# Kernel optimization log

Hardware: AMD Instinct MI355X
Metric: run time of the kernel (lower is better)

## Reference

```python
import jax, jax.numpy as jnp
from jax import lax
import numpy as np

H = 64   # hidden_dim
R = 32   # rank


def setup_inputs() -> dict:
    key = jax.random.key(0)
    ks = jax.random.split(key, 18)
    B, C, T = 64, 256, 512
    s = 0.1
    f32 = jnp.float32
    return {
        "x": jax.random.normal(ks[0], (B, C, T), f32),
        "y": jax.random.normal(ks[1], (B, C, 1), f32),
        # GRU layer 0 (input_size=1)
        "W_ih0": (jax.random.normal(ks[2], (3 * H, 1), f32) * s),
        "W_hh0": (jax.random.normal(ks[3], (3 * H, H), f32) * s),
        "b_ih0": (jax.random.normal(ks[4], (3 * H,), f32) * s),
        "b_hh0": (jax.random.normal(ks[5], (3 * H,), f32) * s),
        # GRU layer 1 (input_size=H)
        "W_ih1": (jax.random.normal(ks[6], (3 * H, H), f32) * s),
        "W_hh1": (jax.random.normal(ks[7], (3 * H, H), f32) * s),
        "b_ih1": (jax.random.normal(ks[8], (3 * H,), f32) * s),
        "b_hh1": (jax.random.normal(ks[9], (3 * H,), f32) * s),
        # heads
        "W_mean": (jax.random.normal(ks[10], (1, H), f32) * s),
        "b_mean": (jax.random.normal(ks[11], (1,), f32) * s),
        "W_d": (jax.random.normal(ks[12], (1, H), f32) * s),
        "b_d": (jax.random.normal(ks[13], (1,), f32) * s),
        "W_v": (jax.random.normal(ks[14], (R, H), f32) * s),
        "b_v": (jax.random.normal(ks[15], (R,), f32) * s),
    }


def _gru_cell(xin, h, Wih, Whh, bih, bhh):
    # PyTorch GRU cell. xin: [N, in], h: [N, H]
    gx = xin @ Wih.T + bih            # [N, 3H]
    gh = h @ Whh.T + bhh              # [N, 3H]
    r = jax.nn.sigmoid(gx[:, :H] + gh[:, :H])
    z = jax.nn.sigmoid(gx[:, H:2 * H] + gh[:, H:2 * H])
    n = jnp.tanh(gx[:, 2 * H:] + r * gh[:, 2 * H:])
    return (1.0 - z) * n + z * h


def reference(x, y, W_ih0, W_hh0, b_ih0, b_hh0, W_ih1, W_hh1, b_ih1, b_hh1,
              W_mean, b_mean, W_d, b_d, W_v, b_v):
    B, C, T = x.shape
    N = B * C
    # Original loops the GRU over channels; channels are independent sequences,
    # so batch them all: [T, N, 1]
    xs = x.reshape(N, T).T[:, :, None]

    def step(carry, xt):
        h0, h1 = carry
        h0 = _gru_cell(xt, h0, W_ih0, W_hh0, b_ih0, b_hh0)
        h1 = _gru_cell(h0, h1, W_ih1, W_hh1, b_ih1, b_hh1)
        return (h0, h1), None

    h0 = jnp.zeros((N, H), x.dtype)
    (_, hT), _ = lax.scan(step, (h0, h0), xs)   # hT: last output of top layer
    hT = hT.reshape(B, C, H)

    mu = hT @ W_mean.T + b_mean                 # [B, C, 1]
    v = hT @ W_v.T + b_v                        # [B, C, R]
    d = jnp.log1p(jnp.exp(hT @ W_d.T + b_d))[..., 0]   # softplus, [B, C]

    sigma = jnp.einsum('bcr,bkr->bck', v, v) + jnp.eye(C, dtype=x.dtype) * d[:, :, None]
    resid = y - mu                              # [B, C, 1]
    inv = jnp.linalg.inv(sigma)
    quad = jnp.einsum('bci,bck,bkj->b', resid, inv, resid)
    logdet = jnp.linalg.slogdet(sigma)[1]
    return jnp.mean(quad + logdet)
```

## Files before the change

### kernel.cpp

```cpp
#include <hip/hip_runtime.h>

typedef __attribute__((ext_vector_type(8))) _Float16 f16x8;
typedef __attribute__((ext_vector_type(4))) float f32x4;

namespace {

constexpr int H_ = 64;
constexpr int R_ = 32;
constexpr int B_ = 64;
constexpr int C_ = 256;
constexpr int T_ = 512;
constexpr int N_ = B_ * C_;

constexpr float NLOG2E  = -1.44269504088896f;
constexpr float N2LOG2E = -2.88539008177793f;

#define MFMA16(a, b, c) __builtin_amdgcn_mfma_f32_16x16x32_f16((a), (b), (c), 0, 0, 0)

__device__ __forceinline__ float gru_combine(float h, float t_n, float t_z) {
    float vn  = 1.0f + t_n;
    float num = __fmaf_rn(h, vn, (1.0f - t_n) * t_z);
    float den = vn * (1.0f + t_z);
    return num * __builtin_amdgcn_rcpf(den);
}

__global__ void pack_weights_kernel(const float* __restrict__ Whh0,
                                    const float* __restrict__ Wih1,
                                    const float* __restrict__ Whh1,
                                    _Float16* __restrict__ packed)
{
    const int b = blockIdx.x;
    const int w = b / 18, f = b % 18;
    const int l = threadIdx.x;
    const int c = l & 15, g = l >> 4;
    const int hb = w * 16;
    const int kk = f & 1;
    const float* src = Whh0;
    int row = 0;
    switch (f >> 1) {
        case 0: src = Whh0; row = hb + c;        break;
        case 1: src = Whh0; row = 64 + hb + c;   break;
        case 2: src = Whh0; row = 128 + hb + c;  break;
        case 3: src = Wih1; row = hb + c;        break;
        case 4: src = Whh1; row = hb + c;        break;
        case 5: src = Wih1; row = 64 + hb + c;   break;
        case 6: src = Whh1; row = 64 + hb + c;   break;
        case 7: src = Wih1; row = 128 + hb + c;  break;
        case 8: src = Whh1; row = 128 + hb + c;  break;
    }
    _Float16* dst = packed + ((size_t)(w * 18 + f) * 512) + (size_t)l * 8;
    #pragma unroll
    for (int j = 0; j < 8; ++j) {
        int k = kk * 32 + g * 8 + j;
        dst[j] = (_Float16)src[row * 64 + k];
    }
}


#define PHASE_L0(PP, DT)                                                      \
  do {                                                                        \
    const _Float16* h0rd = &h0s[(PP) ^ 1][0][0];                              \
    f16x8 a00 = *(const f16x8*)(h0rd + c * 72 + g * 8);                       \
    f16x8 a01 = *(const f16x8*)(h0rd + c * 72 + 32 + g * 8);                  \
    f32x4 accr = MFMA16(a01, Br[1], MFMA16(a00, Br[0], zv));                  \
    f32x4 accz = MFMA16(a01, Br[3], MFMA16(a00, Br[2], zv));                  \
    f32x4 accn = MFMA16(a01, Br[5], MFMA16(a00, Br[4], zv));                  \
    float4 xq = *(const float4*)(&xs_[DT][g * 4]);                            \
    _Pragma("unroll")                                                         \
    for (int q = 0; q < 4; ++q) {                                             \
      int seq = g * 4 + q;                                                    \
      float xv = ((const float*)&xq)[q];                                      \
      float tr = __builtin_amdgcn_exp2f(                                      \
          __fmaf_rn(__fmaf_rn(xv, wr0, accr[q]), NLOG2E, cb0r));              \
      float r  = __builtin_amdgcn_rcpf(1.0f + tr);                            \
      float tz = __builtin_amdgcn_exp2f(                                      \
          __fmaf_rn(__fmaf_rn(xv, wz0, accz[q]), NLOG2E, cb0z));              \
      float pn = __fmaf_rn(r, accn[q] + b0nh, __fmaf_rn(xv, wn0, b0nx));      \
      float tn = __builtin_amdgcn_exp2f(pn * N2LOG2E);                        \
      float hn = gru_combine(h0st[q], tn, tz);                                \
      h0st[q] = hn;                                                           \
      h0s[PP][seq][hid] = (_Float16)hn;                                       \
    }                                                                         \
  } while (0)

#define PHASE_L1(PP, DOSTORE)                                                 \
  do {                                                                        \
    const _Float16* h0rd = &h0s[(PP) ^ 1][0][0];                              \
    const _Float16* h1rd = &h1s[(PP) ^ 1][0][0];                              \
    f16x8 a00 = *(const f16x8*)(h0rd + c * 72 + g * 8);                       \
    f16x8 a01 = *(const f16x8*)(h0rd + c * 72 + 32 + g * 8);                  \
    f16x8 ah0 = *(const f16x8*)(h1rd + c * 72 + g * 8);                       \
    f16x8 ah1 = *(const f16x8*)(h1rd + c * 72 + 32 + g * 8);                  \
    f32x4 r1  = MFMA16(ah1, Br[3], MFMA16(ah0, Br[2],                         \
                MFMA16(a01, Br[1], MFMA16(a00, Br[0], zv))));                 \
    f32x4 z1  = MFMA16(ah1, Br[7], MFMA16(ah0, Br[6],                         \
                MFMA16(a01, Br[5], MFMA16(a00, Br[4], zv))));                 \
    f32x4 xn1 = MFMA16(a01, Br[9],  MFMA16(a00, Br[8],  zv));                 \
    f32x4 hn1 = MFMA16(ah1, Br[11], MFMA16(ah0, Br[10], zv));                 \
    _Pragma("unroll")                                                         \
    for (int q = 0; q < 4; ++q) {                                             \
      int seq = g * 4 + q;                                                    \
      float tr = __builtin_amdgcn_exp2f(__fmaf_rn(r1[q], NLOG2E, cb1r));      \
      float r  = __builtin_amdgcn_rcpf(1.0f + tr);                            \
      float tz = __builtin_amdgcn_exp2f(__fmaf_rn(z1[q], NLOG2E, cb1z));      \
      float pn = __fmaf_rn(r, hn1[q] + b1nh, xn1[q] + b1nx);                  \
      float tn = __builtin_amdgcn_exp2f(pn * N2LOG2E);                        \
      float hn = gru_combine(h1st[q], tn, tz);                                \
      h1st[q] = hn;                                                           \
      if (DOSTORE) h1s[PP][seq][hid] = (_Float16)hn;                          \
    }                                                                         \
  } while (0)

__global__ __launch_bounds__(512, 4)
void gru_mfma_kernel(const float* __restrict__ x,
                     const _Float16* __restrict__ packedW,
                     const float* __restrict__ Wih0,
                     const float* __restrict__ bih0,
                     const float* __restrict__ bhh0,
                     const float* __restrict__ bih1,
                     const float* __restrict__ bhh1,
                     float* __restrict__ hT_out)
{
    __shared__ __align__(16) _Float16 h0s[2][16][72];
    __shared__ __align__(16) _Float16 h1s[2][16][72];
    __shared__ __align__(16) float xs_[32][20];

    const int tid = threadIdx.x;
    const int l = tid & 63;
    const int w = tid >> 6;
    const bool isL0 = (w < 4);
    const int sl = isL0 ? w : (w - 4);
    const int c = l & 15, g = (l >> 4) & 3;
    const int hid = sl * 16 + c;
    const int n0 = blockIdx.x * 16;

    f16x8 Br[12];
    {
        const f16x8* bp = (const f16x8*)(packedW + (size_t)sl * 18 * 512);
        if (isL0) {
            #pragma unroll
            for (int f = 0; f < 6; ++f) Br[f] = bp[f * 64 + l];
        } else {
            #pragma unroll
            for (int f = 0; f < 12; ++f) Br[f] = bp[(6 + f) * 64 + l];
        }
    }

    float wr0 = 0.f, wz0 = 0.f, wn0 = 0.f, cb0r = 0.f, cb0z = 0.f;
    float b0nh = 0.f, b0nx = 0.f, cb1r = 0.f, cb1z = 0.f, b1nx = 0.f, b1nh = 0.f;
    if (isL0) {
        wr0 = Wih0[hid]; wz0 = Wih0[64 + hid]; wn0 = Wih0[128 + hid];
        cb0r = NLOG2E * (bhh0[hid] + bih0[hid]);
        cb0z = NLOG2E * (bhh0[64 + hid] + bih0[64 + hid]);
        b0nh = bhh0[128 + hid];
        b0nx = bih0[128 + hid];
    } else {
        cb1r = NLOG2E * (bih1[hid] + bhh1[hid]);
        cb1z = NLOG2E * (bih1[64 + hid] + bhh1[64 + hid]);
        b1nx = bih1[128 + hid];
        b1nh = bhh1[128 + hid];
    }

    for (int p = tid; p < 2 * 16 * 72; p += 512) {
        (&h0s[0][0][0])[p] = (_Float16)0.0f;
        (&h1s[0][0][0])[p] = (_Float16)0.0f;
    }
    float h0st[4] = {0.f, 0.f, 0.f, 0.f};
    float h1st[4] = {0.f, 0.f, 0.f, 0.f};

    auto stage_x = [&](int t0) {
        int tb = tid & 31;
        int ss = tid >> 5;
        xs_[tb][ss] = x[(size_t)(n0 + ss) * T_ + t0 + tb];
    };

    const f32x4 zv = {0.f, 0.f, 0.f, 0.f};

    stage_x(0);
    __syncthreads();
    if (isL0) PHASE_L0(0, 0);

    for (int p = 1; p < T_ - 1; p += 2) {
        __syncthreads();
        if (isL0) PHASE_L0(1, p & 31); else PHASE_L1(1, true);
        if (((p + 1) & 31) == 0) {
            __syncthreads();
            stage_x(p + 1);
        }
        __syncthreads();
        if (isL0) PHASE_L0(0, (p + 1) & 31); else PHASE_L1(0, true);
    }

    __syncthreads();
    if (isL0) PHASE_L0(1, 31); else PHASE_L1(1, true);

    __syncthreads();
    if (!isL0) {
        PHASE_L1(0, false);
        #pragma unroll
        for (int q = 0; q < 4; ++q) {
            int seq = g * 4 + q;
            hT_out[(size_t)(n0 + seq) * H_ + hid] = h1st[q];
        }
    }
}

__global__ __launch_bounds__(256)
void heads_kernel(const float* __restrict__ hT,
                  const float* __restrict__ y,
                  const float* __restrict__ Wm, const float* __restrict__ bm,
                  const float* __restrict__ Wd, const float* __restrict__ bd,
                  const float* __restrict__ Wv, const float* __restrict__ bv,
                  float* __restrict__ v_out,
                  float* __restrict__ dd_out,
                  float* __restrict__ r_out)
{
    const int n = blockIdx.x * 256 + threadIdx.x;
    const float* h = hT + (size_t)n * H_;

    float hreg[H_];
    #pragma unroll
    for (int j = 0; j < H_; j += 4) {
        float4 q = *(const float4*)(h + j);
        hreg[j] = q.x; hreg[j + 1] = q.y; hreg[j + 2] = q.z; hreg[j + 3] = q.w;
    }
    float mu = bm[0], dv = bd[0];
    #pragma unroll
    for (int j = 0; j < H_; ++j) {
        mu = __fmaf_rn(Wm[j], hreg[j], mu);
        dv = __fmaf_rn(Wd[j], hreg[j], dv);
    }
    r_out[n]  = y[n] - mu;
    dd_out[n] = log1pf(__expf(dv));

    for (int k = 0; k < R_; ++k) {
        float acc = bv[k];
        #pragma unroll
        for (int j = 0; j < H_; ++j)
            acc = __fmaf_rn(Wv[k * H_ + j], hreg[j], acc);
        v_out[(size_t)n * R_ + k] = acc;
    }
}

__device__ __forceinline__ float block_reduce_sum256(float* red, int tid, float val)
{
    red[tid] = val;
    __syncthreads();
    for (int off = 128; off > 0; off >>= 1) {
        if (tid < off) red[tid] += red[tid + off];
        __syncthreads();
    }
    float r = red[0];
    __syncthreads();
    return r;
}

__global__ __launch_bounds__(256)
void woodbury_kernel(const float* __restrict__ v_in,
                     const float* __restrict__ dd_in,
                     const float* __restrict__ r_in,
                     float* __restrict__ batch_out)
{
    __shared__ float Vl[C_][R_ + 1];
    __shared__ float Vw[C_][R_ + 1];
    __shared__ float wi[C_];
    __shared__ float rl[C_];
    __shared__ float red[256];
    __shared__ float MA[R_][R_ + 1];
    __shared__ float uA[R_], yA[R_], wA[R_];

    const int tid = threadIdx.x;
    const int nb  = blockIdx.x * C_;

    for (int p = tid; p < C_ * R_; p += 256) {
        int cc = p >> 5, k = p & 31;
        Vl[cc][k] = v_in[(size_t)(nb + cc) * R_ + k];
    }
    float dval = dd_in[nb + tid];
    float winv = 1.0f / dval;
    float rv   = r_in[nb + tid];
    wi[tid] = winv;
    rl[tid] = rv;
    __syncthreads();

    for (int p = tid; p < C_ * R_; p += 256) {
        int cc = p >> 5, k = p & 31;
        Vw[cc][k] = Vl[cc][k] * wi[cc];
    }
    __syncthreads();

    float slogd = block_reduce_sum256(red, tid, __logf(dval));
    float rDr   = block_reduce_sum256(red, tid, rv * rv * winv);

    #pragma unroll
    for (int e = 0; e < 4; ++e) {
        int p = tid + e * 256;
        int i = p >> 5, j = p & 31;
        float acc = (i == j) ? 1.0f : 0.0f;
        for (int cc = 0; cc < C_; ++cc)
            acc = __fmaf_rn(Vw[cc][i], Vl[cc][j], acc);
        MA[i][j] = acc;
    }
    if (tid < R_) {
        float acc = 0.0f;
        for (int cc = 0; cc < C_; ++cc)
            acc = __fmaf_rn(Vw[cc][tid], rl[cc], acc);
        uA[tid] = acc;
    }
    __syncthreads();

    for (int k = 0; k < R_; ++k) {
        if (tid == 0) MA[k][k] = sqrtf(MA[k][k]);
        __syncthreads();
        if (tid > k && tid < R_) MA[tid][k] /= MA[k][k];
        __syncthreads();
        if (tid > k && tid < R_) {
            float ljk = MA[tid][k];
            for (int i2 = k + 1; i2 <= tid; ++i2)
                MA[tid][i2] -= ljk * MA[i2][k];
        }
        __syncthreads();
    }
    float ldm = block_reduce_sum256(red, tid,
                    (tid < R_) ? 2.0f * __logf(MA[tid][tid]) : 0.0f);

    if (tid == 0) {
        for (int k = 0; k < R_; ++k) {
            float sv = uA[k];
            for (int i2 = 0; i2 < k; ++i2) sv -= MA[k][i2] * yA[i2];
            yA[k] = sv / MA[k][k];
        }
        for (int k = R_ - 1; k >= 0; --k) {
            float sv = yA[k];
            for (int i2 = k + 1; i2 < R_; ++i2) sv -= MA[i2][k] * wA[i2];
            wA[k] = sv / MA[k][k];
        }
        float uw = 0.0f;
        for (int k = 0; k < R_; ++k) uw += wA[k] * uA[k];
        batch_out[blockIdx.x] = (rDr - uw) + slogd + ldm;
    }
}

__global__ void finalize_kernel(const float* __restrict__ bws, float* __restrict__ out)
{
    float v = bws[threadIdx.x];
    #pragma unroll
    for (int off = 32; off > 0; off >>= 1)
        v += __shfl_down(v, off, 64);
    if (threadIdx.x == 0) out[0] = v * (1.0f / 64.0f);
}

}

extern "C" void kernel_launch(void* const* d_in, const int* in_sizes, int n_in,
                              void* d_out, int out_size, void* d_ws, size_t ws_size,
                              hipStream_t stream)
{
    const float* x    = (const float*)d_in[0];
    const float* y    = (const float*)d_in[1];
    const float* Wih0 = (const float*)d_in[2];
    const float* Whh0 = (const float*)d_in[3];
    const float* bih0 = (const float*)d_in[4];
    const float* bhh0 = (const float*)d_in[5];
    const float* Wih1 = (const float*)d_in[6];
    const float* Whh1 = (const float*)d_in[7];
    const float* bih1 = (const float*)d_in[8];
    const float* bhh1 = (const float*)d_in[9];
    const float* Wm   = (const float*)d_in[10];
    const float* bm   = (const float*)d_in[11];
    const float* Wd   = (const float*)d_in[12];
    const float* bd   = (const float*)d_in[13];
    const float* Wv   = (const float*)d_in[14];
    const float* bv   = (const float*)d_in[15];

    char* ws = (char*)d_ws;
    float*    hT     = (float*)(ws + 0);
    float*    v_ws   = (float*)(ws + 4194304);
    float*    dd_ws  = (float*)(ws + 6291456);
    float*    r_ws   = (float*)(ws + 6356992);
    float*    b_ws   = (float*)(ws + 6422528);
    _Float16* packed = (_Float16*)(ws + 6423552);

    pack_weights_kernel<<<72, 64, 0, stream>>>(Whh0, Wih1, Whh1, packed);
    gru_mfma_kernel<<<N_ / 16, 512, 0, stream>>>(
        x, packed, Wih0, bih0, bhh0, bih1, bhh1, hT);
    heads_kernel<<<N_ / 256, 256, 0, stream>>>(
        hT, y, Wm, bm, Wd, bd, Wv, bv, v_ws, dd_ws, r_ws);
    woodbury_kernel<<<B_, 256, 0, stream>>>(v_ws, dd_ws, r_ws, b_ws);
    finalize_kernel<<<1, 64, 0, stream>>>(b_ws, (float*)d_out);
}
```

Baseline: 1.029 ms.

## Double-buffer x staging, fold tanh scale into weights, prioritize MFMA issue

The x staging buffer is double-buffered, which removes one extra __syncthreads per 32 timesteps in the serial recurrence. The -2*log2(e) factor of the n-gate is folded into the packed fp16 weights and biases, saving a multiply per element. s_setprio raises wave priority around the MFMA chains. Pre-scaling the weights before fp16 conversion slightly changes rounding.

```diff
diff --git a/kernel.cpp b/kernel.cpp
--- a/kernel.cpp
+++ b/kernel.cpp
@@ -37,35 +37,38 @@
     const int kk = f & 1;
     const float* src = Whh0;
     int row = 0;
+    float scale = 1.0f;
     switch (f >> 1) {
         case 0: src = Whh0; row = hb + c;        break;
         case 1: src = Whh0; row = 64 + hb + c;   break;
-        case 2: src = Whh0; row = 128 + hb + c;  break;
+        case 2: src = Whh0; row = 128 + hb + c;  scale = N2LOG2E; break;
         case 3: src = Wih1; row = hb + c;        break;
         case 4: src = Whh1; row = hb + c;        break;
         case 5: src = Wih1; row = 64 + hb + c;   break;
         case 6: src = Whh1; row = 64 + hb + c;   break;
-        case 7: src = Wih1; row = 128 + hb + c;  break;
-        case 8: src = Whh1; row = 128 + hb + c;  break;
+        case 7: src = Wih1; row = 128 + hb + c;  scale = N2LOG2E; break;
+        case 8: src = Whh1; row = 128 + hb + c;  scale = N2LOG2E; break;
     }
     _Float16* dst = packed + ((size_t)(w * 18 + f) * 512) + (size_t)l * 8;
     #pragma unroll
     for (int j = 0; j < 8; ++j) {
         int k = kk * 32 + g * 8 + j;
-        dst[j] = (_Float16)src[row * 64 + k];
-    }
-}
-
-
-#define PHASE_L0(PP, DT)                                                      \
+        dst[j] = (_Float16)(src[row * 64 + k] * scale);
+    }
+}
+
+
+#define PHASE_L0(PP, XB, DT)                                                  \
   do {                                                                        \
     const _Float16* h0rd = &h0s[(PP) ^ 1][0][0];                              \
     f16x8 a00 = *(const f16x8*)(h0rd + c * 72 + g * 8);                       \
     f16x8 a01 = *(const f16x8*)(h0rd + c * 72 + 32 + g * 8);                  \
+    __builtin_amdgcn_s_setprio(1);                                            \
     f32x4 accr = MFMA16(a01, Br[1], MFMA16(a00, Br[0], zv));                  \
     f32x4 accz = MFMA16(a01, Br[3], MFMA16(a00, Br[2], zv));                  \
     f32x4 accn = MFMA16(a01, Br[5], MFMA16(a00, Br[4], zv));                  \
-    float4 xq = *(const float4*)(&xs_[DT][g * 4]);                            \
+    __builtin_amdgcn_s_setprio(0);                                            \
+    float4 xq = *(const float4*)(&xs_[XB][DT][g * 4]);                        \
     _Pragma("unroll")                                                         \
     for (int q = 0; q < 4; ++q) {                                             \
       int seq = g * 4 + q;                                                    \
@@ -75,8 +78,8 @@
       float r  = __builtin_amdgcn_rcpf(1.0f + tr);                            \
       float tz = __builtin_amdgcn_exp2f(                                      \
           __fmaf_rn(__fmaf_rn(xv, wz0, accz[q]), NLOG2E, cb0z));              \
-      float pn = __fmaf_rn(r, accn[q] + b0nh, __fmaf_rn(xv, wn0, b0nx));      \
-      float tn = __builtin_amdgcn_exp2f(pn * N2LOG2E);                        \
+      float tn = __builtin_amdgcn_exp2f(                                      \
+          __fmaf_rn(r, accn[q] + b0nh, __fmaf_rn(xv, wn0, b0nx)));            \
       float hn = gru_combine(h0st[q], tn, tz);                                \
       h0st[q] = hn;                                                           \
       h0s[PP][seq][hid] = (_Float16)hn;                                       \
@@ -91,20 +94,22 @@
     f16x8 a01 = *(const f16x8*)(h0rd + c * 72 + 32 + g * 8);                  \
     f16x8 ah0 = *(const f16x8*)(h1rd + c * 72 + g * 8);                       \
     f16x8 ah1 = *(const f16x8*)(h1rd + c * 72 + 32 + g * 8);                  \
+    __builtin_amdgcn_s_setprio(1);                                            \
     f32x4 r1  = MFMA16(ah1, Br[3], MFMA16(ah0, Br[2],                         \
                 MFMA16(a01, Br[1], MFMA16(a00, Br[0], zv))));                 \
     f32x4 z1  = MFMA16(ah1, Br[7], MFMA16(ah0, Br[6],                         \
                 MFMA16(a01, Br[5], MFMA16(a00, Br[4], zv))));                 \
     f32x4 xn1 = MFMA16(a01, Br[9],  MFMA16(a00, Br[8],  zv));                 \
     f32x4 hn1 = MFMA16(ah1, Br[11], MFMA16(ah0, Br[10], zv));                 \
+    __builtin_amdgcn_s_setprio(0);                                            \
     _Pragma("unroll")                                                         \
     for (int q = 0; q < 4; ++q) {                                             \
       int seq = g * 4 + q;                                                    \
       float tr = __builtin_amdgcn_exp2f(__fmaf_rn(r1[q], NLOG2E, cb1r));      \
       float r  = __builtin_amdgcn_rcpf(1.0f + tr);                            \
       float tz = __builtin_amdgcn_exp2f(__fmaf_rn(z1[q], NLOG2E, cb1z));      \
-      float pn = __fmaf_rn(r, hn1[q] + b1nh, xn1[q] + b1nx);                  \
-      float tn = __builtin_amdgcn_exp2f(pn * N2LOG2E);                        \
+      float tn = __builtin_amdgcn_exp2f(                                      \
+          __fmaf_rn(r, hn1[q] + b1nh, xn1[q] + b1nx));                        \
       float hn = gru_combine(h1st[q], tn, tz);                                \
       h1st[q] = hn;                                                           \
       if (DOSTORE) h1s[PP][seq][hid] = (_Float16)hn;                          \
@@ -123,7 +128,7 @@
 {
     __shared__ __align__(16) _Float16 h0s[2][16][72];
     __shared__ __align__(16) _Float16 h1s[2][16][72];
-    __shared__ __align__(16) float xs_[32][20];
+    __shared__ __align__(16) float xs_[2][32][20];
 
     const int tid = threadIdx.x;
     const int l = tid & 63;
@@ -149,16 +154,17 @@
     float wr0 = 0.f, wz0 = 0.f, wn0 = 0.f, cb0r = 0.f, cb0z = 0.f;
     float b0nh = 0.f, b0nx = 0.f, cb1r = 0.f, cb1z = 0.f, b1nx = 0.f, b1nh = 0.f;
     if (isL0) {
-        wr0 = Wih0[hid]; wz0 = Wih0[64 + hid]; wn0 = Wih0[128 + hid];
+        wr0 = Wih0[hid]; wz0 = Wih0[64 + hid];
+        wn0 = N2LOG2E * Wih0[128 + hid];
         cb0r = NLOG2E * (bhh0[hid] + bih0[hid]);
         cb0z = NLOG2E * (bhh0[64 + hid] + bih0[64 + hid]);
-        b0nh = bhh0[128 + hid];
-        b0nx = bih0[128 + hid];
+        b0nh = N2LOG2E * bhh0[128 + hid];
+        b0nx = N2LOG2E * bih0[128 + hid];
     } else {
         cb1r = NLOG2E * (bih1[hid] + bhh1[hid]);
         cb1z = NLOG2E * (bih1[64 + hid] + bhh1[64 + hid]);
-        b1nx = bih1[128 + hid];
-        b1nh = bhh1[128 + hid];
+        b1nx = N2LOG2E * bih1[128 + hid];
+        b1nh = N2LOG2E * bhh1[128 + hid];
     }
 
     for (int p = tid; p < 2 * 16 * 72; p += 512) {
@@ -169,30 +175,29 @@
     float h1st[4] = {0.f, 0.f, 0.f, 0.f};
 
     auto stage_x = [&](int t0) {
+        int buf = (t0 >> 5) & 1;
         int tb = tid & 31;
         int ss = tid >> 5;
-        xs_[tb][ss] = x[(size_t)(n0 + ss) * T_ + t0 + tb];
+        xs_[buf][tb][ss] = x[(size_t)(n0 + ss) * T_ + t0 + tb];
     };
 
     const f32x4 zv = {0.f, 0.f, 0.f, 0.f};
 
     stage_x(0);
     __syncthreads();
-    if (isL0) PHASE_L0(0, 0);
+    if (isL0) PHASE_L0(0, 0, 0);
 
     for (int p = 1; p < T_ - 1; p += 2) {
         __syncthreads();
-        if (isL0) PHASE_L0(1, p & 31); else PHASE_L1(1, true);
-        if (((p + 1) & 31) == 0) {
-            __syncthreads();
-            stage_x(p + 1);
-        }
-        __syncthreads();
-        if (isL0) PHASE_L0(0, (p + 1) & 31); else PHASE_L1(0, true);
-    }
-
-    __syncthreads();
-    if (isL0) PHASE_L0(1, 31); else PHASE_L1(1, true);
+        if (isL0) PHASE_L0(1, (p >> 5) & 1, p & 31); else PHASE_L1(1, true);
+        if ((p & 31) == 31) stage_x(p + 1);
+        __syncthreads();
+        if (isL0) PHASE_L0(0, ((p + 1) >> 5) & 1, (p + 1) & 31);
+        else      PHASE_L1(0, true);
+    }
+
+    __syncthreads();
+    if (isL0) PHASE_L0(1, 1, 31); else PHASE_L1(1, true);
 
     __syncthreads();
     if (!isL0) {
```

New measurement: 978.1 us. 1.05x faster.
